# Performance work log

Measured on AMD Instinct MI355X. Metric: run time of the kernel, lower is better.

## Reference

```python
import jax, jax.numpy as jnp
import numpy as np

F_DIM, P_DIM, H_DIM, N_EXP = 768, 512, 1024, 4
B, T = 8192, 8192


def _gelu(x):
    return jax.nn.gelu(x, approximate=False)


def _normalize(x, eps=1e-12):
    n = jnp.linalg.norm(x, axis=-1, keepdims=True)
    return x / jnp.maximum(n, eps)


def setup_inputs() -> dict:
    key = jax.random.key(0)
    ks = jax.random.split(key, 24)
    s = 0.02
    inp = {
        'image_features': jax.random.normal(ks[0], (B, F_DIM), jnp.float32),
        'text_features': jax.random.normal(ks[1], (B, F_DIM), jnp.float32),
        'target_features': jax.random.normal(ks[2], (T, F_DIM), jnp.float32),
        # projection layers (torch Linear convention: W [out,in])
        'Wt': jax.random.normal(ks[3], (P_DIM, F_DIM), jnp.float32) * s,
        'bt': jnp.zeros((P_DIM,), jnp.float32),
        'Wi': jax.random.normal(ks[4], (P_DIM, F_DIM), jnp.float32) * s,
        'bi': jnp.zeros((P_DIM,), jnp.float32),
        # dynamic scalar MLP: (2P -> H -> 1)
        'ds_W1': jax.random.normal(ks[5], (H_DIM, 2 * P_DIM), jnp.float32) * s,
        'ds_b1': jnp.zeros((H_DIM,), jnp.float32),
        'ds_W2': jax.random.normal(ks[6], (1, H_DIM), jnp.float32) * s,
        'ds_b2': jnp.zeros((1,), jnp.float32),
        # experts stacked: [E, H, 2P]
        'exp_W': jax.random.normal(ks[7], (N_EXP, H_DIM, 2 * P_DIM), jnp.float32) * s,
        'exp_b': jnp.zeros((N_EXP, H_DIM), jnp.float32),
        # router: (2P -> H/4 -> E)
        'rt_W1': jax.random.normal(ks[8], (H_DIM // 4, 2 * P_DIM), jnp.float32) * s,
        'rt_b1': jnp.zeros((H_DIM // 4,), jnp.float32),
        'rt_W2': jax.random.normal(ks[9], (N_EXP, H_DIM // 4), jnp.float32) * s,
        'rt_b2': jnp.zeros((N_EXP,), jnp.float32),
        # output layer: (H -> F)
        'out_W': jax.random.normal(ks[10], (F_DIM, H_DIM), jnp.float32) * s,
        'out_b': jnp.zeros((F_DIM,), jnp.float32),
        'logit_scale': jnp.asarray(np.log(50.0), jnp.float32),
    }
    return inp


def reference(image_features, text_features, target_features, Wt, bt, Wi, bi,
              ds_W1, ds_b1, ds_W2, ds_b2, exp_W, exp_b,
              rt_W1, rt_b1, rt_W2, rt_b2, out_W, out_b, logit_scale):
    # eval mode: all dropouts are identity, no modality drop
    tp = _gelu(text_features @ Wt.T + bt)            # [B,P]
    ip = _gelu(image_features @ Wi.T + bi)           # [B,P]
    comb = jnp.concatenate([tp, ip], axis=-1)        # [B,2P]

    router_logits = _gelu(comb @ rt_W1.T + rt_b1) @ rt_W2.T + rt_b2  # [B,E]
    router_probs = jax.nn.softmax(router_logits, axis=-1)

    expert_out = _gelu(jnp.einsum('bd,ehd->beh', comb, exp_W) + exp_b)  # [B,E,H]
    fused_hidden = jnp.einsum('be,beh->bh', router_probs, expert_out)   # [B,H]
    residual = fused_hidden @ out_W.T + out_b                            # [B,F]

    ds = jax.nn.sigmoid(_gelu(comb @ ds_W1.T + ds_b1) @ ds_W2.T + ds_b2)  # [B,1]
    output = ds * text_features + (1.0 - ds) * image_features + residual
    pred = _normalize(output)
    tgt = _normalize(target_features)
    logits = jnp.exp(logit_scale) * (pred @ tgt.T)   # [B,T]
    return (logits, ds, router_probs)
```

## Files before the change

kernel.cpp:

```cpp
#include <hip/hip_runtime.h>
#include <stdint.h>
#include <math.h>

#define BDIM 8192
#define TDIM 8192
#define FDIM 768
#define PDIM 512
#define HDIM 1024
#define NEXP 4
#define NCAT 5376

using short4v = __attribute__((ext_vector_type(4))) short;
using short8 = __attribute__((ext_vector_type(8))) short;
using f32x4  = __attribute__((ext_vector_type(4))) float;

__device__ __forceinline__ short f2bf(float f) {
  uint32_t u = __builtin_bit_cast(uint32_t, f);
  u += 0x7fffu + ((u >> 16) & 1u);
  return (short)(u >> 16);
}
__device__ __forceinline__ float bf2f(short s) {
  uint32_t u = ((uint32_t)(uint16_t)s) << 16;
  return __builtin_bit_cast(float, u);
}
__device__ __forceinline__ float gelu_exact(float x) {
  return 0.5f * x * (1.0f + erff(x * 0.70710678118654752f));
}

#define GLDS(gp, lp) __builtin_amdgcn_global_load_lds( \
    (const __attribute__((address_space(1))) void*)(gp), \
    (__attribute__((address_space(3))) void*)(lp), 16, 0, 0)

template <int MODE>
__device__ __forceinline__ void gemm_body(
    const short* __restrict__ A, int lda,
    const short* __restrict__ B, int ldb,
    void* __restrict__ C, int ldc, int K,
    const float* __restrict__ bias, float scale,
    int m0, int n0)
{
  __shared__ short sA[4096];
  __shared__ short sB[4096];
  const int t    = threadIdx.x;
  const int lane = t & 63;
  const int wave = t >> 6;
  const int wm = (wave >> 1) * 64;
  const int wn = (wave & 1) * 64;
  const int l15  = lane & 15;
  const int quad = lane >> 4;

  f32x4 acc[4][4];
#pragma unroll
  for (int i = 0; i < 4; ++i)
#pragma unroll
    for (int j = 0; j < 4; ++j)
      acc[i][j] = (f32x4){0.f, 0.f, 0.f, 0.f};

  const int rr = t >> 2;
  const int cc = (t & 3) * 8;
  const short* gA0 = A + (size_t)(m0 + rr) * lda + cc;
  const short* gA1 = A + (size_t)(m0 + 64 + rr) * lda + cc;
  const short* gB0 = B + (size_t)(n0 + rr) * ldb + cc;
  const short* gB1 = B + (size_t)(n0 + 64 + rr) * ldb + cc;
  short* lA0 = sA + t * 8;
  short* lA1 = sA + 2048 + t * 8;
  short* lB0 = sB + t * 8;
  short* lB1 = sB + 2048 + t * 8;

  for (int k0 = 0; k0 < K; k0 += 32) {
    GLDS(gA0 + k0, lA0);
    GLDS(gA1 + k0, lA1);
    GLDS(gB0 + k0, lB0);
    GLDS(gB1 + k0, lB1);
    __syncthreads();
    short8 af[4], bfr[4];
#pragma unroll
    for (int i = 0; i < 4; ++i)
      af[i] = *(const short8*)(sA + (wm + i * 16 + l15) * 32 + quad * 8);
#pragma unroll
    for (int j = 0; j < 4; ++j)
      bfr[j] = *(const short8*)(sB + (wn + j * 16 + l15) * 32 + quad * 8);
#pragma unroll
    for (int i = 0; i < 4; ++i)
#pragma unroll
      for (int j = 0; j < 4; ++j)
        acc[i][j] = __builtin_amdgcn_mfma_f32_16x16x32_bf16(af[i], bfr[j], acc[i][j], 0, 0, 0);
    __syncthreads();
  }

#pragma unroll
  for (int i = 0; i < 4; ++i) {
#pragma unroll
    for (int j = 0; j < 4; ++j) {
      const int col = n0 + wn + j * 16 + l15;
      float bv = (MODE == 2) ? 0.f : bias[col];
#pragma unroll
      for (int r = 0; r < 4; ++r) {
        const int row = m0 + wm + i * 16 + quad * 4 + r;
        float v = acc[i][j][r];
        if (MODE == 0) {
          v = gelu_exact(v + bv);
          ((short*)C)[(size_t)row * ldc + col] = f2bf(v);
        } else if (MODE == 1) {
          ((float*)C)[(size_t)row * ldc + col] = v + bv;
        } else {
          ((float*)C)[(size_t)row * ldc + col] = v * scale;
        }
      }
    }
  }
}

template <int MODE>
__global__ __launch_bounds__(256, 2)
void gemm_bt(const short* __restrict__ A, int lda,
             const short* __restrict__ B, int ldb,
             void* __restrict__ C, int ldc, int K,
             const float* __restrict__ bias,
             const float* __restrict__ scale_ptr)
{
  float scale = 1.f;
  if (MODE == 2) scale = expf(scale_ptr[0]);
  gemm_body<MODE>(A, lda, B, ldb, C, ldc, K, bias, scale,
                  blockIdx.y * 128, blockIdx.x * 128);
}

__global__ __launch_bounds__(256, 2)
void gemm_proj(const short* __restrict__ textb, const short* __restrict__ imgb,
               const short* __restrict__ Wtb, const short* __restrict__ Wib,
               const float* __restrict__ bt, const float* __restrict__ bi,
               short* __restrict__ comb)
{
  const int z = blockIdx.z;
  const short* A = z ? imgb : textb;
  const short* B = z ? Wib : Wtb;
  const float* bias = z ? bi : bt;
  short* C = comb + (z ? 512 : 0);
  gemm_body<0>(A, FDIM, B, FDIM, C, 1024, FDIM, bias, 1.f,
               blockIdx.y * 128, blockIdx.x * 128);
}

#define SEG0 1572864u
#define SEG1 3145728u
#define SEG2 3244032u
#define SEG3 3342336u
#define SEG4 4390912u
#define SEG5 4653056u
#define SEG6 4718592u
#define SEG7 4915200u
#define SEG8 4916544u

__global__ __launch_bounds__(256)
void prep_all(const float* __restrict__ text, const float* __restrict__ image,
              const float* __restrict__ Wt, const float* __restrict__ Wi,
              const float* __restrict__ exp_W, const float* __restrict__ ds_W1,
              const float* __restrict__ rt_W1, const float* __restrict__ out_W,
              const float* __restrict__ exp_b, const float* __restrict__ ds_b1,
              const float* __restrict__ rt_b1,
              short* __restrict__ textb, short* __restrict__ imgb,
              short* __restrict__ Wtb, short* __restrict__ Wib,
              short* __restrict__ Bcat, short* __restrict__ outWb,
              float* __restrict__ biascat)
{
  const uint32_t i = blockIdx.x * 256 + threadIdx.x;
  if (i >= SEG8) return;
  if (i >= SEG7) {
    const uint32_t j = (i - SEG7) * 4;
#pragma unroll
    for (int k = 0; k < 4; ++k) {
      uint32_t idx = j + k;
      float v;
      if (idx < 4096)      v = exp_b[idx];
      else if (idx < 5120) v = ds_b1[idx - 4096];
      else                 v = rt_b1[idx - 5120];
      biascat[idx] = v;
    }
    return;
  }
  const float* s;
  short* d;
  uint32_t j;
  if (i < SEG1) {
    if (i < SEG0) { j = i;        s = text;  d = textb; }
    else          { j = i - SEG0; s = image; d = imgb;  }
  } else if (i < SEG3) {
    if (i < SEG2) { j = i - SEG1; s = Wt; d = Wtb; }
    else          { j = i - SEG2; s = Wi; d = Wib; }
  } else if (i < SEG5) {
    if (i < SEG4) { j = i - SEG3; s = exp_W; d = Bcat; }
    else          { j = i - SEG4; s = ds_W1; d = Bcat + (size_t)4096 * 1024; }
  } else {
    if (i < SEG6) { j = i - SEG5; s = rt_W1; d = Bcat + (size_t)5120 * 1024; }
    else          { j = i - SEG6; s = out_W; d = outWb; }
  }
  float4 v = ((const float4*)s)[j];
  short4v o = { f2bf(v.x), f2bf(v.y), f2bf(v.z), f2bf(v.w) };
  ((short4v*)d)[j] = o;
}

__global__ __launch_bounds__(256)
void moe_mix(const short* __restrict__ Hall,
             const float* __restrict__ rt_W2, const float* __restrict__ rt_b2,
             const float* __restrict__ ds_W2, const float* __restrict__ ds_b2,
             float* __restrict__ out_probs, float* __restrict__ out_ds,
             short* __restrict__ fused)
{
  const int b = blockIdx.x;
  const int t = threadIdx.x;
  const int lane = t & 63;
  const int wave = t >> 6;
  const short* h = Hall + (size_t)b * NCAT;

  float rv = bf2f(h[5120 + t]);
  float p0 = rv * rt_W2[t];
  float p1 = rv * rt_W2[256 + t];
  float p2 = rv * rt_W2[512 + t];
  float p3 = rv * rt_W2[768 + t];
  float dd = 0.f;
#pragma unroll
  for (int k = 0; k < 4; ++k)
    dd += bf2f(h[4096 + k * 256 + t]) * ds_W2[k * 256 + t];

#pragma unroll
  for (int off = 32; off; off >>= 1) {
    p0 += __shfl_xor(p0, off);
    p1 += __shfl_xor(p1, off);
    p2 += __shfl_xor(p2, off);
    p3 += __shfl_xor(p3, off);
    dd += __shfl_xor(dd, off);
  }
  __shared__ float red[5][4];
  __shared__ float bc[5];
  if (lane == 0) {
    red[0][wave] = p0; red[1][wave] = p1; red[2][wave] = p2;
    red[3][wave] = p3; red[4][wave] = dd;
  }
  __syncthreads();
  if (t == 0) {
    float l0 = red[0][0] + red[0][1] + red[0][2] + red[0][3] + rt_b2[0];
    float l1 = red[1][0] + red[1][1] + red[1][2] + red[1][3] + rt_b2[1];
    float l2 = red[2][0] + red[2][1] + red[2][2] + red[2][3] + rt_b2[2];
    float l3 = red[3][0] + red[3][1] + red[3][2] + red[3][3] + rt_b2[3];
    float d  = red[4][0] + red[4][1] + red[4][2] + red[4][3] + ds_b2[0];
    float mx = fmaxf(fmaxf(l0, l1), fmaxf(l2, l3));
    float e0 = expf(l0 - mx), e1 = expf(l1 - mx);
    float e2 = expf(l2 - mx), e3 = expf(l3 - mx);
    float inv = 1.f / (e0 + e1 + e2 + e3);
    bc[0] = e0 * inv; bc[1] = e1 * inv; bc[2] = e2 * inv; bc[3] = e3 * inv;
    bc[4] = 1.f / (1.f + expf(-d));
    out_probs[b * 4 + 0] = bc[0];
    out_probs[b * 4 + 1] = bc[1];
    out_probs[b * 4 + 2] = bc[2];
    out_probs[b * 4 + 3] = bc[3];
    out_ds[b] = bc[4];
  }
  __syncthreads();
  const float q0 = bc[0], q1 = bc[1], q2 = bc[2], q3 = bc[3];
  short* fr = fused + (size_t)b * 1024;
#pragma unroll
  for (int c = t; c < 1024; c += 256) {
    float v = q0 * bf2f(h[c])        + q1 * bf2f(h[1024 + c])
            + q2 * bf2f(h[2048 + c]) + q3 * bf2f(h[3072 + c]);
    fr[c] = f2bf(v);
  }
}

__global__ __launch_bounds__(256)
void normalize_both(const float* __restrict__ text, const float* __restrict__ image,
                    const float* __restrict__ ds, const float* __restrict__ resid,
                    const float* __restrict__ target,
                    short* __restrict__ pred, short* __restrict__ tgtb)
{
  const int bb = blockIdx.x;
  const int t = threadIdx.x;
  float o0, o1, o2;
  short* d;
  if (bb < BDIM) {
    const float dv = ds[bb];
    const float* tx = text + (size_t)bb * FDIM;
    const float* im = image + (size_t)bb * FDIM;
    const float* s  = resid + (size_t)bb * FDIM;
    o0 = dv * tx[t]       + (1.f - dv) * im[t]       + s[t];
    o1 = dv * tx[t + 256] + (1.f - dv) * im[t + 256] + s[t + 256];
    o2 = dv * tx[t + 512] + (1.f - dv) * im[t + 512] + s[t + 512];
    d = pred + (size_t)bb * FDIM;
  } else {
    const int b = bb - BDIM;
    const float* s = target + (size_t)b * FDIM;
    o0 = s[t]; o1 = s[t + 256]; o2 = s[t + 512];
    d = tgtb + (size_t)b * FDIM;
  }
  float ss = o0 * o0 + o1 * o1 + o2 * o2;
  __shared__ float red[4];
#pragma unroll
  for (int off = 32; off; off >>= 1) ss += __shfl_xor(ss, off);
  if ((t & 63) == 0) red[t >> 6] = ss;
  __syncthreads();
  const float tot = red[0] + red[1] + red[2] + red[3];
  const float rn = 1.f / fmaxf(sqrtf(tot), 1e-12f);
  d[t]       = f2bf(o0 * rn);
  d[t + 256] = f2bf(o1 * rn);
  d[t + 512] = f2bf(o2 * rn);
}

extern "C" void kernel_launch(void* const* d_in, const int* in_sizes, int n_in,
                              void* d_out, int out_size, void* d_ws, size_t ws_size,
                              hipStream_t stream) {
  const float* image  = (const float*)d_in[0];
  const float* text   = (const float*)d_in[1];
  const float* target = (const float*)d_in[2];
  const float* Wt     = (const float*)d_in[3];
  const float* bt     = (const float*)d_in[4];
  const float* Wi     = (const float*)d_in[5];
  const float* bi     = (const float*)d_in[6];
  const float* ds_W1  = (const float*)d_in[7];
  const float* ds_b1  = (const float*)d_in[8];
  const float* ds_W2  = (const float*)d_in[9];
  const float* ds_b2  = (const float*)d_in[10];
  const float* exp_W  = (const float*)d_in[11];
  const float* exp_b  = (const float*)d_in[12];
  const float* rt_W1  = (const float*)d_in[13];
  const float* rt_b1  = (const float*)d_in[14];
  const float* rt_W2  = (const float*)d_in[15];
  const float* rt_b2  = (const float*)d_in[16];
  const float* out_W  = (const float*)d_in[17];
  const float* out_b  = (const float*)d_in[18];
  const float* logit_scale = (const float*)d_in[19];

  char* ws = (char*)d_ws;
  short* comb  = (short*)ws;  ws += (size_t)BDIM * 1024 * 2;
  short* Hall  = (short*)ws;  ws += (size_t)BDIM * NCAT * 2;
  short* fused = (short*)ws;  ws += (size_t)BDIM * 1024 * 2;
  float* resid = (float*)ws;  ws += (size_t)BDIM * FDIM * 4;
  short* pred  = (short*)ws;  ws += (size_t)BDIM * FDIM * 2;
  short* tgtb  = (short*)ws;  ws += (size_t)TDIM * FDIM * 2;
  short* textb = (short*)ws;  ws += (size_t)BDIM * FDIM * 2;
  short* imgb  = (short*)ws;  ws += (size_t)BDIM * FDIM * 2;
  short* Wtb   = (short*)ws;  ws += (size_t)PDIM * FDIM * 2;
  short* Wib   = (short*)ws;  ws += (size_t)PDIM * FDIM * 2;
  short* outWb = (short*)ws;  ws += (size_t)FDIM * HDIM * 2;
  short* Bcat  = (short*)ws;  ws += (size_t)NCAT * HDIM * 2;
  float* biascat = (float*)ws; ws += (size_t)NCAT * 4;

  float* out_logits = (float*)d_out;
  float* out_ds     = out_logits + (size_t)BDIM * TDIM;
  float* out_probs  = out_ds + BDIM;

  prep_all<<<(SEG8 + 255) / 256, 256, 0, stream>>>(
      text, image, Wt, Wi, exp_W, ds_W1, rt_W1, out_W,
      exp_b, ds_b1, rt_b1,
      textb, imgb, Wtb, Wib, Bcat, outWb, biascat);

  dim3 blk(256);
  gemm_proj<<<dim3(PDIM / 128, BDIM / 128, 2), blk, 0, stream>>>(
      textb, imgb, Wtb, Wib, bt, bi, comb);
  gemm_bt<0><<<dim3(NCAT / 128, BDIM / 128), blk, 0, stream>>>(
      comb, 1024, Bcat, 1024, Hall, NCAT, 1024, biascat, nullptr);
  moe_mix<<<BDIM, 256, 0, stream>>>(Hall, rt_W2, rt_b2, ds_W2, ds_b2,
                                    out_probs, out_ds, fused);
  gemm_bt<1><<<dim3(FDIM / 128, BDIM / 128), blk, 0, stream>>>(
      fused, 1024, outWb, 1024, resid, FDIM, 1024, out_b, nullptr);
  normalize_both<<<BDIM + TDIM, 256, 0, stream>>>(
      text, image, out_ds, resid, target, pred, tgtb);
  gemm_bt<2><<<dim3(TDIM / 128, BDIM / 128), blk, 0, stream>>>(
      pred, FDIM, tgtb, FDIM, out_logits, TDIM, FDIM, nullptr, logit_scale);
}
```

Before: 667.7 us.

## Add 256x256-tile bf16 MFMA GEMM with 4-stage LDS pipeline for big GEMMs

Introduces a new 512-thread GEMM kernel with 256x256 output tiles, a 4-deep global_load_lds ring buffer with XOR-swizzled LDS layout, split A/B staging interleaved with MFMA work, and s_setprio around the math. It replaces the 128x128 GEMM for the expert/router/ds concatenated GEMM and the final logits GEMM. The aim is more data reuse per tile and better overlap of loads with compute. In exchange it uses 128 KB of LDS and many accumulator registers, which limits occupancy, and the 5376/256 = 21 column tiles give fewer blocks and coarser load balance.

```diff
diff --git a/kernel.cpp b/kernel.cpp
--- a/kernel.cpp
+++ b/kernel.cpp
@@ -30,6 +30,133 @@
 #define GLDS(gp, lp) __builtin_amdgcn_global_load_lds( \
     (const __attribute__((address_space(1))) void*)(gp), \
     (__attribute__((address_space(3))) void*)(lp), 16, 0, 0)
+
+template <int MODE>
+__global__ __launch_bounds__(512, 2)
+void gemm256(const short* __restrict__ A, int lda,
+             const short* __restrict__ B, int ldb,
+             void* __restrict__ C, int ldc, int K,
+             const float* __restrict__ bias,
+             const float* __restrict__ scale_ptr)
+{
+  __shared__ short lds_s[65536];
+  const int t    = threadIdx.x;
+  const int lane = t & 63;
+  const int wave = t >> 6;
+  const int wr   = wave >> 2;
+  const int wc   = wave & 3;
+  const int l15  = lane & 15;
+  const int quad = lane >> 4;
+  const int m0 = blockIdx.y * 256;
+  const int n0 = blockIdx.x * 256;
+  const int NT = K >> 5;
+
+  float scale = 1.f;
+  if (MODE == 2) scale = expf(scale_ptr[0]);
+
+  const uint32_t Sl   = (uint32_t)t * 16u;
+  const uint32_t Ssw  = Sl ^ (((Sl >> 7) & 7u) << 4);
+  const uint32_t srow = Ssw >> 6;
+  const uint32_t sk   = ((Ssw >> 4) & 3u) * 8u;
+  const short* gA0 = A + (size_t)(m0 + srow) * lda + sk;
+  const short* gA1 = A + (size_t)(m0 + 128 + srow) * lda + sk;
+  const short* gB0 = B + (size_t)(n0 + srow) * ldb + sk;
+  const short* gB1 = B + (size_t)(n0 + 128 + srow) * ldb + sk;
+  short* lp = lds_s + t * 8;
+
+#define STAGE_A(kt) { const int tb = ((kt) & 3) << 14; const int kk = (kt) << 5; \
+    GLDS(gA0 + kk, lp + tb); GLDS(gA1 + kk, lp + tb + 4096); }
+#define STAGE_B(kt) { const int tb = ((kt) & 3) << 14; const int kk = (kt) << 5; \
+    GLDS(gB0 + kk, lp + tb + 8192); GLDS(gB1 + kk, lp + tb + 12288); }
+
+  int offA[8], offB[4];
+#pragma unroll
+  for (int x = 0; x < 8; ++x) {
+    uint32_t S = (uint32_t)((wr * 128 + (x >> 2) * 64 + (x & 3) * 16 + l15) * 64 + quad * 16);
+    offA[x] = (int)((S ^ (((S >> 7) & 7u) << 4)) >> 1);
+  }
+#pragma unroll
+  for (int j = 0; j < 4; ++j) {
+    uint32_t S = (uint32_t)((wc * 64 + j * 16 + l15) * 64 + quad * 16);
+    offB[j] = (int)(((S ^ (((S >> 7) & 7u) << 4)) >> 1) + 8192u);
+  }
+
+  f32x4 acc[8][4];
+#pragma unroll
+  for (int i = 0; i < 8; ++i)
+#pragma unroll
+    for (int j = 0; j < 4; ++j)
+      acc[i][j] = (f32x4){0.f, 0.f, 0.f, 0.f};
+
+  STAGE_A(0); STAGE_B(0);
+  if (NT > 1) { STAGE_A(1); STAGE_B(1); }
+  if (NT > 2) { STAGE_A(2); STAGE_B(2); }
+  if (NT > 2)      asm volatile("s_waitcnt vmcnt(8)" ::: "memory");
+  else if (NT > 1) asm volatile("s_waitcnt vmcnt(4)" ::: "memory");
+  else             asm volatile("s_waitcnt vmcnt(0)" ::: "memory");
+  asm volatile("s_barrier" ::: "memory");
+
+  for (int kt = 0; kt < NT; ++kt) {
+    const short* tile = lds_s + ((kt & 3) << 14);
+    short8 a[4], b[4];
+    if (kt + 3 < NT) { STAGE_A(kt + 3); }
+#pragma unroll
+    for (int j = 0; j < 4; ++j) b[j] = *(const short8*)(tile + offB[j]);
+#pragma unroll
+    for (int i = 0; i < 4; ++i) a[i] = *(const short8*)(tile + offA[i]);
+    __builtin_amdgcn_s_setprio(1);
+#pragma unroll
+    for (int i = 0; i < 4; ++i)
+#pragma unroll
+      for (int j = 0; j < 4; ++j)
+        acc[i][j] = __builtin_amdgcn_mfma_f32_16x16x32_bf16(a[i], b[j], acc[i][j], 0, 0, 0);
+    __builtin_amdgcn_s_setprio(0);
+    asm volatile("s_barrier" ::: "memory");
+    if (kt + 3 < NT) { STAGE_B(kt + 3); }
+#pragma unroll
+    for (int i = 0; i < 4; ++i) a[i] = *(const short8*)(tile + offA[4 + i]);
+    __builtin_amdgcn_s_setprio(1);
+#pragma unroll
+    for (int i = 0; i < 4; ++i)
+#pragma unroll
+      for (int j = 0; j < 4; ++j)
+        acc[4 + i][j] = __builtin_amdgcn_mfma_f32_16x16x32_bf16(a[i], b[j], acc[4 + i][j], 0, 0, 0);
+    __builtin_amdgcn_s_setprio(0);
+    if (kt < NT - 1) {
+      if (kt + 3 < NT)      asm volatile("s_waitcnt vmcnt(8) lgkmcnt(0)" ::: "memory");
+      else if (kt + 2 < NT) asm volatile("s_waitcnt vmcnt(4) lgkmcnt(0)" ::: "memory");
+      else                  asm volatile("s_waitcnt vmcnt(0) lgkmcnt(0)" ::: "memory");
+      asm volatile("s_barrier" ::: "memory");
+    }
+  }
+#undef STAGE_A
+#undef STAGE_B
+
+#pragma unroll
+  for (int mh = 0; mh < 2; ++mh) {
+#pragma unroll
+    for (int i = 0; i < 4; ++i) {
+      const int rowb = m0 + wr * 128 + mh * 64 + i * 16 + quad * 4;
+#pragma unroll
+      for (int j = 0; j < 4; ++j) {
+        const int col = n0 + wc * 64 + j * 16 + l15;
+        const float bv = (MODE == 2) ? 0.f : bias[col];
+        f32x4 v = acc[mh * 4 + i][j];
+#pragma unroll
+        for (int r = 0; r < 4; ++r) {
+          float x = v[r];
+          if (MODE == 0) {
+            ((short*)C)[(size_t)(rowb + r) * ldc + col] = f2bf(gelu_exact(x + bv));
+          } else if (MODE == 1) {
+            ((float*)C)[(size_t)(rowb + r) * ldc + col] = x + bv;
+          } else {
+            ((float*)C)[(size_t)(rowb + r) * ldc + col] = x * scale;
+          }
+        }
+      }
+    }
+  }
+}
 
 template <int MODE>
 __device__ __forceinline__ void gemm_body(
@@ -354,7 +481,7 @@
   dim3 blk(256);
   gemm_proj<<<dim3(PDIM / 128, BDIM / 128, 2), blk, 0, stream>>>(
       textb, imgb, Wtb, Wib, bt, bi, comb);
-  gemm_bt<0><<<dim3(NCAT / 128, BDIM / 128), blk, 0, stream>>>(
+  gemm256<0><<<dim3(NCAT / 256, BDIM / 256), dim3(512), 0, stream>>>(
       comb, 1024, Bcat, 1024, Hall, NCAT, 1024, biascat, nullptr);
   moe_mix<<<BDIM, 256, 0, stream>>>(Hall, rt_W2, rt_b2, ds_W2, ds_b2,
                                     out_probs, out_ds, fused);
@@ -362,6 +489,6 @@
       fused, 1024, outWb, 1024, resid, FDIM, 1024, out_b, nullptr);
   normalize_both<<<BDIM + TDIM, 256, 0, stream>>>(
       text, image, out_ds, resid, target, pred, tgtb);
-  gemm_bt<2><<<dim3(TDIM / 128, BDIM / 128), blk, 0, stream>>>(
+  gemm256<2><<<dim3(TDIM / 256, BDIM / 256), dim3(512), 0, stream>>>(
       pred, FDIM, tgtb, FDIM, out_logits, TDIM, FDIM, nullptr, logit_scale);
 }
```

Measured after the change: 673.4 us. About the same (+0.9%).
